# Optimization experiments

Hardware: AMD Instinct MI355X
Metric: run time of the kernel (lower is better)

The kernel has to match this reference:

```python
import jax, jax.numpy as jnp
import numpy as np

N, E, D, T = 50000, 800000, 64, 4
FI = D // T   # per-tower input features (divide_input=True)
FO = D // T   # per-tower output features (output_dim // towers)
NAGG, NSC = 4, 3  # mean/min/max/std ; identity/amplification/attenuation
AVG_LOG = float(np.log(17.0))  # from deg histogram: all nodes have degree 16


def setup_inputs() -> dict:
    key = jax.random.key(0)
    ks = jax.random.split(key, 12)
    rn = lambda k, s: jax.random.normal(k, s, dtype=jnp.float32) * 0.1
    z = lambda s: jnp.zeros(s, jnp.float32)
    post_in = (1 + NAGG * NSC) * FI  # cat([x, scaled aggregations]) per tower
    return {
        "x": jax.random.normal(ks[0], (N, D), dtype=jnp.float32),
        "edge_index": jax.random.randint(ks[1], (2, E), 0, N),
        "alpha": jnp.full((1,), 0.5, dtype=jnp.float32),
        "lin_self_W": rn(ks[2], (D, D)), "lin_self_b": z((D,)),
        "pre_W_s2d": rn(ks[3], (T, 2 * FI, FI)), "pre_b_s2d": z((T, FI)),
        "post_W_s2d": rn(ks[4], (T, post_in, FO)), "post_b_s2d": z((T, FO)),
        "lin_W_s2d": rn(ks[5], (T * FO, D)), "lin_b_s2d": z((D,)),
        "pre_W_d2s": rn(ks[6], (T, 2 * FI, FI)), "pre_b_d2s": z((T, FI)),
        "post_W_d2s": rn(ks[7], (T, post_in, FO)), "post_b_d2s": z((T, FO)),
        "lin_W_d2s": rn(ks[8], (T * FO, D)), "lin_b_d2s": z((D,)),
    }


def _pna(x, recv, send, preW, preb, postW, postb, linW, linb):
    """One PNAConv: messages from `send` nodes aggregated at `recv` nodes."""
    n = x.shape[0]
    xt = x.reshape(n, T, FI)
    # message: per tower cat(x_i, x_j) -> single pre layer (pre_layers=1)
    h = jnp.concatenate([xt[recv], xt[send]], axis=-1)          # [E, T, 2*FI]
    m = jnp.einsum('etf,tfg->etg', h, preW) + preb              # [E, T, FI]
    # aggregators: mean, min, max, std (scatter-reduce over receiver)
    cnt = jax.ops.segment_sum(jnp.ones((recv.shape[0],), m.dtype), recv, n)
    deg = jnp.maximum(cnt, 1.0)[:, None, None]                  # clamp(1), as PyG
    mean = jax.ops.segment_sum(m, recv, n) / deg
    mean_sq = jax.ops.segment_sum(m * m, recv, n) / deg
    std = jnp.sqrt(jnp.maximum(mean_sq - mean * mean, 0.0) + 1e-5)
    has = (cnt > 0.0)[:, None, None]
    mn = jnp.where(has, jax.ops.segment_min(m, recv, n), 0.0)
    mx = jnp.where(has, jax.ops.segment_max(m, recv, n), 0.0)
    agg = jnp.concatenate([mean, mn, mx, std], axis=-1)         # [n, T, 4*FI]
    # degree scalers: identity, amplification, attenuation
    amp = jnp.log(deg + 1.0) / AVG_LOG
    out = jnp.concatenate([agg, agg * amp, agg / amp], axis=-1)  # [n, T, 12*FI]
    out = jnp.concatenate([xt, out], axis=-1)                   # [n, T, 13*FI]
    out = jnp.einsum('ntf,tfg->ntg', out, postW) + postb        # [n, T, FO]
    return out.reshape(n, T * FO) @ linW + linb                 # [n, D]


def reference(x, edge_index, alpha, lin_self_W, lin_self_b,
              pre_W_s2d, pre_b_s2d, post_W_s2d, post_b_s2d, lin_W_s2d, lin_b_s2d,
              pre_W_d2s, pre_b_d2s, post_W_d2s, post_b_d2s, lin_W_d2s, lin_b_d2s):
    src, dst = edge_index[0], edge_index[1]
    y_self = x @ lin_self_W + lin_self_b
    # flow='source_to_target': x_j = src, aggregated at dst
    y_s2d = _pna(x, dst, src, pre_W_s2d, pre_b_s2d, post_W_s2d, post_b_s2d, lin_W_s2d, lin_b_s2d)
    # flow='target_to_source': x_j = dst, aggregated at src
    y_d2s = _pna(x, src, dst, pre_W_d2s, pre_b_d2s, post_W_d2s, post_b_d2s, lin_W_d2s, lin_b_d2s)
    a = alpha[0]
    return y_self + (1.0 - a) * y_s2d + a * y_d2s
```

## Files before the change

### kernel.cpp

```cpp
#include <hip/hip_runtime.h>
#include <math.h>


typedef _Float16 half_t;
typedef __attribute__((ext_vector_type(8))) _Float16 half8;
typedef __attribute__((ext_vector_type(2))) _Float16 half2v;
typedef __attribute__((ext_vector_type(4))) float f32x4;

#define FCAP 12288

static __device__ __forceinline__ unsigned pkmin(unsigned a, unsigned b) {
    unsigned r;
    asm("v_pk_min_f16 %0, %1, %2" : "=v"(r) : "v"(a), "v"(b));
    return r;
}
static __device__ __forceinline__ unsigned pkmax(unsigned a, unsigned b) {
    unsigned r;
    asm("v_pk_max_f16 %0, %1, %2" : "=v"(r) : "v"(a), "v"(b));
    return r;
}
static __device__ __forceinline__ int h2i(half2v h) { return __builtin_bit_cast(int, h); }
static __device__ __forceinline__ half2v u2h(unsigned i) { return __builtin_bit_cast(half2v, i); }
static __device__ __forceinline__ half2v pkrtz(float a, float b) {
    return __builtin_bit_cast(half2v, __builtin_amdgcn_cvt_pkrtz(a, b));
}

__global__ __launch_bounds__(256) void k_pre(
    const int* __restrict__ ei, int nE, int nN,
    int* __restrict__ histD, int* __restrict__ histS,
    const float* __restrict__ postW1, const float* __restrict__ postW2,
    const float* __restrict__ linW1, const float* __restrict__ linW2,
    const float* __restrict__ Wself, const float* __restrict__ bself,
    const float* __restrict__ linb1, const float* __restrict__ linb2,
    const float* __restrict__ postb1, const float* __restrict__ postb2,
    const float* __restrict__ alpha,
    half_t* __restrict__ WLg, half_t* __restrict__ WfinTg, float* __restrict__ bfin,
    const float* __restrict__ x,
    const float* __restrict__ preW1, const float* __restrict__ preW2,
    const float* __restrict__ preb1, const float* __restrict__ preb2,
    half_t* __restrict__ P1, half_t* __restrict__ P2,
    half_t* __restrict__ Q1, half_t* __restrict__ Q2, half_t* __restrict__ xh) {
    int tid = threadIdx.x;
    int b = blockIdx.x;
    if (b < 256) {
        __shared__ int hD[256], hS[256];
        hD[tid] = 0; hS[tid] = 0;
        __syncthreads();
        int chunk = (nE + 255) >> 8;
        int lo = b * chunk;
        int hi = lo + chunk; if (hi > nE) hi = nE;
        for (int e = lo + tid; e < hi; e += 256) {
            int s = ei[e], d = ei[nE + e];
            atomicAdd(&hD[d >> 8], 1);
            atomicAdd(&hS[s >> 8], 1);
        }
        __syncthreads();
        histD[tid * 256 + b] = hD[tid];
        histS[tid * 256 + b] = hS[tid];
    } else if (b < 320) {
        const float a = alpha[0];
        int id = (b - 256) * 256 + tid;
        const int stride = 64 * 256;
        for (int i = id; i < 24 * 16 * 72; i += stride) {
            int m = i / (16 * 72);
            int r = i % (16 * 72);
            int go = r / 72, k = r % 72;
            int d = m / 12, t = (m / 3) % 4, mat = m % 3;
            float v = 0.f;
            if (k < 64) {
                int stat = k >> 4, g = k & 15;
                int basep = (mat == 0) ? 1 : (mat == 1 ? 5 : 9);
                const float* pw = d ? postW2 : postW1;
                v = pw[t * 3328 + ((basep + stat) * 16 + g) * 16 + go];
            }
            WLg[i] = (half_t)v;
        }
        for (int i = id; i < 64 * 192; i += stride) {
            int o = i / 192, k = i % 192;
            float v;
            if (k < 64)       v = (1.f - a) * linW1[k * 64 + o];
            else if (k < 128) v = a * linW2[(k - 64) * 64 + o];
            else {
                int kx = k - 128, t = kx >> 4, f = kx & 15;
                v = Wself[kx * 64 + o];
                float s1 = 0.f, s2 = 0.f;
                for (int go = 0; go < 16; ++go) {
                    s1 += postW1[t * 3328 + f * 16 + go] * linW1[(t * 16 + go) * 64 + o];
                    s2 += postW2[t * 3328 + f * 16 + go] * linW2[(t * 16 + go) * 64 + o];
                }
                v += (1.f - a) * s1 + a * s2;
            }
            WfinTg[i] = (half_t)v;
        }
        for (int i = id; i < 64; i += stride) {
            float v = bself[i] + (1.f - a) * linb1[i] + a * linb2[i];
            for (int j = 0; j < 64; ++j)
                v += (1.f - a) * postb1[j] * linW1[j * 64 + i]
                   + a * postb2[j] * linW2[j * 64 + i];
            bfin[i] = v;
        }
    } else {
        int vb = b - 320;
        const int lane = tid & 63;
        const int t = lane >> 4, g = lane & 15;
        const int base = t << 4;
        float wsP1[16], wsP2[16], wsQ1[16], wsQ2[16];
#pragma unroll
        for (int f = 0; f < 16; ++f) {
            wsP1[f] = preW1[t * 512 + (16 + f) * 16 + g];
            wsP2[f] = preW2[t * 512 + (16 + f) * 16 + g];
            wsQ1[f] = preW1[t * 512 + f * 16 + g];
            wsQ2[f] = preW2[t * 512 + f * 16 + g];
        }
        const float pb1 = preb1[lane], pb2 = preb2[lane];
        int node = (vb * 256 + tid) >> 6;
        const int stride = (768 * 256) >> 6;
        for (; node < nN; node += stride) {
            float xv = x[(size_t)node * 64 + lane];
            float p1 = 0.f, p2 = 0.f, q1 = pb1, q2 = pb2;
#pragma unroll
            for (int f = 0; f < 16; ++f) {
                float v = __shfl(xv, base + f, 64);
                p1 = fmaf(v, wsP1[f], p1);
                p2 = fmaf(v, wsP2[f], p2);
                q1 = fmaf(v, wsQ1[f], q1);
                q2 = fmaf(v, wsQ2[f], q2);
            }
            size_t o = (size_t)node * 64 + lane;
            P1[o] = (half_t)p1;
            P2[o] = (half_t)p2;
            Q1[o] = (half_t)q1;
            Q2[o] = (half_t)q2;
            xh[o] = (half_t)xv;
        }
    }
}

__global__ __launch_bounds__(256) void k_scanA(
    const int* __restrict__ cnt0, const int* __restrict__ cnt1,
    int* __restrict__ off0, int* __restrict__ off1,
    int* __restrict__ bsum, int n, int nchunk) {
    int arr = blockIdx.x >= nchunk;
    int c = blockIdx.x - (arr ? nchunk : 0);
    const int* cnt = arr ? cnt1 : cnt0;
    int* off = arr ? off1 : off0;
    int tid = threadIdx.x;
    int base = c * 1024 + tid * 4;
    int v[4];
#pragma unroll
    for (int k = 0; k < 4; ++k) { int i = base + k; v[k] = (i < n) ? cnt[i] : 0; }
    int tsum = v[0] + v[1] + v[2] + v[3];
    int lane = tid & 63, wid = tid >> 6;
    int incl = tsum;
#pragma unroll
    for (int d = 1; d < 64; d <<= 1) {
        int t = __shfl_up(incl, d, 64);
        if (lane >= d) incl += t;
    }
    __shared__ int ws[4];
    if (lane == 63) ws[wid] = incl;
    __syncthreads();
    int wpre = 0;
    for (int ww = 0; ww < wid; ++ww) wpre += ws[ww];
    int e = wpre + incl - tsum;
#pragma unroll
    for (int k = 0; k < 4; ++k) { int i = base + k; if (i < n) off[i] = e; e += v[k]; }
    if (tid == 255) bsum[blockIdx.x] = wpre + incl;
}

__global__ __launch_bounds__(256) void k_scanB(
    int* __restrict__ off0, int* __restrict__ off1,
    const int* __restrict__ bsum, int n, int nchunk) {
    int arr = blockIdx.x >= nchunk;
    int c = blockIdx.x - (arr ? nchunk : 0);
    int* off = arr ? off1 : off0;
    const int* bs = bsum + (arr ? nchunk : 0);
    __shared__ int pre_s, tot_s;
    int tid = threadIdx.x;
    if (tid < 64) {
        int v = (tid < nchunk) ? bs[tid] : 0;
        int incl = v;
#pragma unroll
        for (int d = 1; d < 64; d <<= 1) {
            int t = __shfl_up(incl, d, 64);
            if (tid >= d) incl += t;
        }
        if (tid == c) pre_s = incl - v;
        if (tid == nchunk - 1) tot_s = incl;
    }
    __syncthreads();
    int pre = pre_s;
    int base = c * 1024 + tid * 4;
#pragma unroll
    for (int k = 0; k < 4; ++k) {
        int i = base + k;
        if (i < n) off[i] += pre;
    }
    if (c == 0 && tid == 0) off[n] = tot_s;
}

__global__ __launch_bounds__(256) void k_bin(
    const int* __restrict__ ei, int nE, int nbuck,
    const int* __restrict__ curD, const int* __restrict__ curS,
    unsigned* __restrict__ binnedD, unsigned* __restrict__ binnedS) {
    __shared__ int cD[256], cS[256];
    int tid = threadIdx.x;
    int hb = blockIdx.x;
    if (tid < nbuck) {
        cD[tid] = curD[tid * 256 + hb];
        cS[tid] = curS[tid * 256 + hb];
    }
    __syncthreads();
    int chunk = (nE + 255) >> 8;
    int lo = hb * chunk;
    int hi = lo + chunk; if (hi > nE) hi = nE;
    for (int e = lo + tid; e < hi; e += 256) {
        int s = ei[e], d = ei[nE + e];
        unsigned pk = (unsigned)s | ((unsigned)d << 16);
        int p = atomicAdd(&cD[d >> 8], 1);
        binnedD[p] = pk;
        int q = atomicAdd(&cS[s >> 8], 1);
        binnedS[q] = pk;
    }
}

__global__ __launch_bounds__(256) void k_fine(
    const unsigned* __restrict__ binnedD, const unsigned* __restrict__ binnedS,
    const int* __restrict__ curD, const int* __restrict__ curS,
    int* __restrict__ off_dst, int* __restrict__ off_src,
    unsigned short* __restrict__ adj_dst, unsigned short* __restrict__ adj_src,
    int nE, int nN, int nbuck) {
    int bk = blockIdx.x;
    int dd = 0;
    if (bk >= nbuck) { dd = 1; bk -= nbuck; }
    const unsigned* binned = dd ? binnedS : binnedD;
    const int* cur = dd ? curS : curD;
    int* off = dd ? off_src : off_dst;
    unsigned short* adj = dd ? adj_src : adj_dst;
    __shared__ int ncnt[256];
    __shared__ int cur2[256];
    __shared__ unsigned short stage[FCAP];
    int tid = threadIdx.x;
    ncnt[tid] = 0;
    __syncthreads();
    int base = cur[bk * 256];
    int endp = cur[(bk + 1) * 256];
    int cntE = endp - base;
    int n0 = bk << 8;
    for (int i = tid; i < cntE; i += 256) {
        unsigned pk = binned[base + i];
        int key = dd ? (int)(pk & 0xFFFFu) : (int)(pk >> 16);
        atomicAdd(&ncnt[key - n0], 1);
    }
    __syncthreads();
    if (tid < 64) {
        int i4 = tid << 2;
        int v0 = ncnt[i4], v1 = ncnt[i4 + 1], v2 = ncnt[i4 + 2], v3 = ncnt[i4 + 3];
        int tsum = v0 + v1 + v2 + v3;
        int incl = tsum;
#pragma unroll
        for (int d = 1; d < 64; d <<= 1) {
            int t = __shfl_up(incl, d, 64);
            if (tid >= d) incl += t;
        }
        int excl = incl - tsum;
        ncnt[i4] = excl;
        ncnt[i4 + 1] = excl + v0;
        ncnt[i4 + 2] = excl + v0 + v1;
        ncnt[i4 + 3] = excl + v0 + v1 + v2;
    }
    __syncthreads();
    cur2[tid] = ncnt[tid];
    int node = n0 + tid;
    if (node < nN) off[node] = base + ncnt[tid];
    if (bk == nbuck - 1 && tid == 0) off[nN] = nE;
    __syncthreads();
    for (int i = tid; i < cntE; i += 256) {
        unsigned pk = binned[base + i];
        int key = dd ? (int)(pk & 0xFFFFu) : (int)(pk >> 16);
        int oth = dd ? (int)(pk >> 16) : (int)(pk & 0xFFFFu);
        int pos = atomicAdd(&cur2[key - n0], 1);
        if (pos < FCAP) stage[pos] = (unsigned short)oth;
        else adj[base + pos] = (unsigned short)oth;
    }
    __syncthreads();
    int lim = cntE < FCAP ? cntE : FCAP;
    for (int i = tid; i < lim; i += 256) adj[base + i] = stage[i];
}

__global__ __launch_bounds__(256) void k_gather(
    const half_t* __restrict__ P1, const half_t* __restrict__ P2,
    const half_t* __restrict__ Q1, const half_t* __restrict__ Q2,
    const int* __restrict__ off1, const unsigned short* __restrict__ adj1,
    const int* __restrict__ off2, const unsigned short* __restrict__ adj2,
    half_t* __restrict__ agg1, half_t* __restrict__ agg2,
    float* __restrict__ amp1, float* __restrict__ ramp1,
    float* __restrict__ amp2, float* __restrict__ ramp2, int nN, int nE) {
    int tid = threadIdx.x;
    const int lane = tid & 63;
    const int g = lane >> 4;
    const int fl = lane & 15;
    const int fl8 = fl << 3;
    int w4 = (blockIdx.x * 256 + tid) >> 6;
    int wstride = (gridDim.x * 256) >> 6;
    int ngroups = (nN + 3) >> 2;
#pragma unroll
    for (int d = 0; d < 2; ++d) {
        const char* Pc = (const char*)(d ? P2 : P1);
        const char* Qc = (const char*)(d ? Q2 : Q1);
        const int* off = d ? off2 : off1;
        const unsigned short* adj = d ? adj2 : adj1;
        char* aggc = (char*)(d ? agg2 : agg1);
        float* ampA = d ? amp2 : amp1;
        float* rampA = d ? ramp2 : ramp1;
        for (int gi = w4; gi < ngroups; gi += wstride) {
            int node = gi * 4 + g;
            bool act = node < nN;
            int nodec = act ? node : (nN - 1);
            int beg = off[nodec], end = off[nodec + 1];
            int cnt = end - beg;
            half2v s01 = {(half_t)0, (half_t)0}, s23 = {(half_t)0, (half_t)0};
            half2v ss01 = {(half_t)0, (half_t)0}, ss23 = {(half_t)0, (half_t)0};
            unsigned mn0 = 0x7C007C00u, mn1 = 0x7C007C00u;
            unsigned mx0 = 0xFC00FC00u, mx1 = 0xFC00FC00u;
            int j = beg;
            for (; j + 4 <= end; j += 4) {
                int n0 = adj[j + 0];
                int n1 = adj[j + 1];
                int n2 = adj[j + 2];
                int n3 = adj[j + 3];
                uint2 u0 = *(const uint2*)(Pc + n0 * 128 + fl8);
                uint2 u1 = *(const uint2*)(Pc + n1 * 128 + fl8);
                uint2 u2 = *(const uint2*)(Pc + n2 * 128 + fl8);
                uint2 u3 = *(const uint2*)(Pc + n3 * 128 + fl8);
                half2v a0 = u2h(u0.x), a1 = u2h(u0.y);
                half2v b0 = u2h(u1.x), b1 = u2h(u1.y);
                half2v c0 = u2h(u2.x), c1 = u2h(u2.y);
                half2v e0 = u2h(u3.x), e1 = u2h(u3.y);
                s01 += (a0 + b0) + (c0 + e0);
                s23 += (a1 + b1) + (c1 + e1);
                ss01 += a0 * a0; ss23 += a1 * a1;
                ss01 += b0 * b0; ss23 += b1 * b1;
                ss01 += c0 * c0; ss23 += c1 * c1;
                ss01 += e0 * e0; ss23 += e1 * e1;
                mn0 = pkmin(mn0, pkmin(pkmin(u0.x, u1.x), pkmin(u2.x, u3.x)));
                mn1 = pkmin(mn1, pkmin(pkmin(u0.y, u1.y), pkmin(u2.y, u3.y)));
                mx0 = pkmax(mx0, pkmax(pkmax(u0.x, u1.x), pkmax(u2.x, u3.x)));
                mx1 = pkmax(mx1, pkmax(pkmax(u0.y, u1.y), pkmax(u2.y, u3.y)));
            }
            for (; j < end; ++j) {
                int n0 = adj[j];
                uint2 u0 = *(const uint2*)(Pc + n0 * 128 + fl8);
                half2v a0 = u2h(u0.x), a1 = u2h(u0.y);
                s01 += a0; s23 += a1;
                ss01 += a0 * a0; ss23 += a1 * a1;
                mn0 = pkmin(mn0, u0.x); mn1 = pkmin(mn1, u0.y);
                mx0 = pkmax(mx0, u0.x); mx1 = pkmax(mx1, u0.y);
            }
            float deg = (cnt > 0) ? (float)cnt : 1.0f;
            float inv = 1.0f / deg;
            float se0 = (float)s01[0], se1 = (float)s01[1];
            float se2 = (float)s23[0], se3 = (float)s23[1];
            float sq0 = (float)ss01[0], sq1 = (float)ss01[1];
            float sq2 = (float)ss23[0], sq3 = (float)ss23[1];
            float me0 = se0 * inv, me1 = se1 * inv, me2 = se2 * inv, me3 = se3 * inv;
            float st0 = sqrtf(fmaxf(fmaf(-me0, me0, sq0 * inv), 0.f) + 1e-5f);
            float st1 = sqrtf(fmaxf(fmaf(-me1, me1, sq1 * inv), 0.f) + 1e-5f);
            float st2 = sqrtf(fmaxf(fmaf(-me2, me2, sq2 * inv), 0.f) + 1e-5f);
            float st3 = sqrtf(fmaxf(fmaf(-me3, me3, sq3 * inv), 0.f) + 1e-5f);
            uint2 qu = *(const uint2*)(Qc + nodec * 128 + fl8);
            half2v q01 = u2h(qu.x), q23 = u2h(qu.y);
            half2v hm01, hm23, hl01, hl23, hh01, hh23;
            if (cnt > 0) {
                hm01 = q01 + pkrtz(me0, me1);
                hm23 = q23 + pkrtz(me2, me3);
                hl01 = q01 + u2h(mn0); hl23 = q23 + u2h(mn1);
                hh01 = q01 + u2h(mx0); hh23 = q23 + u2h(mx1);
            } else {
                half2v z = {(half_t)0, (half_t)0};
                hm01 = z; hm23 = z; hl01 = z; hl23 = z; hh01 = z; hh23 = z;
            }
            half2v hs01 = pkrtz(st0, st1);
            half2v hs23 = pkrtz(st2, st3);
            if (act) {
                char* ab = aggc + (size_t)node * 512 + (fl >> 2) * 128 + (fl & 3) * 8;
                uint2 w0; w0.x = (unsigned)h2i(hm01); w0.y = (unsigned)h2i(hm23);
                uint2 w1; w1.x = (unsigned)h2i(hl01); w1.y = (unsigned)h2i(hl23);
                uint2 w2; w2.x = (unsigned)h2i(hh01); w2.y = (unsigned)h2i(hh23);
                uint2 w3; w3.x = (unsigned)h2i(hs01); w3.y = (unsigned)h2i(hs23);
                *(uint2*)(ab)      = w0;
                *(uint2*)(ab + 32) = w1;
                *(uint2*)(ab + 64) = w2;
                *(uint2*)(ab + 96) = w3;
                if (fl == 0) {
                    float ampv = __log2f(deg + 1.0f) * 0.24465054f;
                    ampA[node] = ampv;
                    rampA[node] = 1.0f / ampv;
                }
            }
        }
    }
}

__global__ __launch_bounds__(256, 2) void k_c(
    const half_t* __restrict__ xh,
    const half_t* __restrict__ agg1, const half_t* __restrict__ agg2,
    const float* __restrict__ amp1, const float* __restrict__ ramp1,
    const float* __restrict__ amp2, const float* __restrict__ ramp2,
    const half_t* __restrict__ WLg, const half_t* __restrict__ WfinT,
    const float* __restrict__ bfin, float* __restrict__ out, int nN) {
    __shared__ half_t WLs[24 * 16 * 72];
    __shared__ half_t osb[4 * 16 * 72];
    int tid = threadIdx.x;
    {
        const uint4* src = (const uint4*)WLg;
        uint4* dst = (uint4*)WLs;
        for (int i = tid; i < (24 * 16 * 72) / 8; i += 256) dst[i] = src[i];
    }
    __syncthreads();
    int w = tid >> 6, lane = tid & 63;
    int l15 = lane & 15, g4 = lane >> 4;
    half_t* ow = osb + w * (16 * 72) + l15 * 72;
    half8 wfr[4][6];
#pragma unroll
    for (int ct = 0; ct < 4; ++ct)
#pragma unroll
        for (int kk = 0; kk < 6; ++kk)
            wfr[ct][kk] = *(const half8*)(WfinT + (ct * 16 + l15) * 192 + kk * 32 + g4 * 8);
    float4 bf4[4];
#pragma unroll
    for (int ct = 0; ct < 4; ++ct)
        bf4[ct] = *(const float4*)(bfin + ct * 16 + g4 * 4);
    int nwaves = gridDim.x * 4;
    int wgid = blockIdx.x * 4 + w;
    int ntiles = (nN + 15) >> 4;
    for (int tile = wgid; tile < ntiles; tile += nwaves) {
        int nrow = (tile << 4) + l15;
        int nrowc = (nrow < nN) ? nrow : (nN - 1);
        half8 xbf[2];
#pragma unroll
        for (int ks = 0; ks < 2; ++ks)
            xbf[ks] = *(const half8*)(xh + (size_t)nrowc * 64 + ks * 32 + g4 * 8);
        f32x4 accY[4] = {{0,0,0,0},{0,0,0,0},{0,0,0,0},{0,0,0,0}};
#pragma unroll
        for (int d = 0; d < 2; ++d) {
            const half_t* agg = d ? agg2 : agg1;
            float ampv = (d ? amp2 : amp1)[nrowc];
            float rampv = (d ? ramp2 : ramp1)[nrowc];
#pragma unroll
            for (int t = 0; t < 4; ++t) {
                half8 b0 = *(const half8*)(agg + (size_t)nrowc * 256 + t * 64 + g4 * 8);
                half8 b1 = *(const half8*)(agg + (size_t)nrowc * 256 + t * 64 + 32 + g4 * 8);
                const half_t* wb = WLs + ((d * 12 + t * 3) * 16 + l15) * 72 + g4 * 8;
                half8 aA0 = *(const half8*)(wb);
                half8 aA1 = *(const half8*)(wb + 32);
                half8 aB0 = *(const half8*)(wb + 16 * 72);
                half8 aB1 = *(const half8*)(wb + 16 * 72 + 32);
                half8 aE0 = *(const half8*)(wb + 32 * 72);
                half8 aE1 = *(const half8*)(wb + 32 * 72 + 32);
                f32x4 zA = {0,0,0,0}, zB = {0,0,0,0}, zE = {0,0,0,0};
                zA = __builtin_amdgcn_mfma_f32_16x16x32_f16(aA0, b0, zA, 0, 0, 0);
                zA = __builtin_amdgcn_mfma_f32_16x16x32_f16(aA1, b1, zA, 0, 0, 0);
                zB = __builtin_amdgcn_mfma_f32_16x16x32_f16(aB0, b0, zB, 0, 0, 0);
                zB = __builtin_amdgcn_mfma_f32_16x16x32_f16(aB1, b1, zB, 0, 0, 0);
                zE = __builtin_amdgcn_mfma_f32_16x16x32_f16(aE0, b0, zE, 0, 0, 0);
                zE = __builtin_amdgcn_mfma_f32_16x16x32_f16(aE1, b1, zE, 0, 0, 0);
                float o0 = zA[0] + ampv * zB[0] + rampv * zE[0];
                float o1 = zA[1] + ampv * zB[1] + rampv * zE[1];
                float o2 = zA[2] + ampv * zB[2] + rampv * zE[2];
                float o3 = zA[3] + ampv * zB[3] + rampv * zE[3];
                half2v p0; p0[0] = (half_t)o0; p0[1] = (half_t)o1;
                half2v p1; p1[0] = (half_t)o2; p1[1] = (half_t)o3;
                *(half2v*)(ow + t * 16 + g4 * 4) = p0;
                *(half2v*)(ow + t * 16 + g4 * 4 + 2) = p1;
            }
#pragma unroll
            for (int ks = 0; ks < 2; ++ks) {
                half8 ob = *(const half8*)(ow + ks * 32 + g4 * 8);
#pragma unroll
                for (int ct = 0; ct < 4; ++ct)
                    accY[ct] = __builtin_amdgcn_mfma_f32_16x16x32_f16(wfr[ct][d * 2 + ks], ob, accY[ct], 0, 0, 0);
            }
        }
#pragma unroll
        for (int ks = 0; ks < 2; ++ks)
#pragma unroll
            for (int ct = 0; ct < 4; ++ct)
                accY[ct] = __builtin_amdgcn_mfma_f32_16x16x32_f16(wfr[ct][4 + ks], xbf[ks], accY[ct], 0, 0, 0);
        if (nrow < nN) {
#pragma unroll
            for (int ct = 0; ct < 4; ++ct) {
                float4 st;
                st.x = accY[ct][0] + bf4[ct].x;
                st.y = accY[ct][1] + bf4[ct].y;
                st.z = accY[ct][2] + bf4[ct].z;
                st.w = accY[ct][3] + bf4[ct].w;
                *(float4*)(out + (size_t)nrow * 64 + ct * 16 + g4 * 4) = st;
            }
        }
    }
}

extern "C" void kernel_launch(void* const* d_in, const int* in_sizes, int n_in,
                              void* d_out, int out_size, void* d_ws, size_t ws_size,
                              hipStream_t stream) {
    const float* x      = (const float*)d_in[0];
    const int*   ei     = (const int*)d_in[1];
    const float* alpha  = (const float*)d_in[2];
    const float* Wself  = (const float*)d_in[3];
    const float* bself  = (const float*)d_in[4];
    const float* preW1  = (const float*)d_in[5];
    const float* preb1  = (const float*)d_in[6];
    const float* postW1 = (const float*)d_in[7];
    const float* postb1 = (const float*)d_in[8];
    const float* linW1  = (const float*)d_in[9];
    const float* linb1  = (const float*)d_in[10];
    const float* preW2  = (const float*)d_in[11];
    const float* preb2  = (const float*)d_in[12];
    const float* postW2 = (const float*)d_in[13];
    const float* postb2 = (const float*)d_in[14];
    const float* linW2  = (const float*)d_in[15];
    const float* linb2  = (const float*)d_in[16];
    float* out = (float*)d_out;
    const int nN = in_sizes[0] / 64;
    const int nE = in_sizes[1] / 2;
    const int nbuck = (nN + 255) >> 8;
    const int nH = nbuck * 256;
    const int nchunk = (nH + 1023) >> 10;

    char* w = (char*)d_ws;
    size_t ofs = 0;
    auto alloc = [&](size_t bytes) {
        char* p = w + ofs;
        ofs = (ofs + bytes + 255) & ~(size_t)255;
        return p;
    };
    half_t* P1   = (half_t*)alloc((size_t)nN * 64 * 2);
    half_t* P2   = (half_t*)alloc((size_t)nN * 64 * 2);
    half_t* Q1   = (half_t*)alloc((size_t)nN * 64 * 2);
    half_t* Q2   = (half_t*)alloc((size_t)nN * 64 * 2);
    half_t* xh   = (half_t*)alloc((size_t)nN * 64 * 2);
    half_t* agg1 = (half_t*)alloc((size_t)nN * 256 * 2);
    half_t* agg2 = (half_t*)alloc((size_t)nN * 256 * 2);
    float* amp1  = (float*)alloc((size_t)nN * 4);
    float* ramp1 = (float*)alloc((size_t)nN * 4);
    float* amp2  = (float*)alloc((size_t)nN * 4);
    float* ramp2 = (float*)alloc((size_t)nN * 4);
    half_t* WLg   = (half_t*)alloc(24 * 16 * 72 * 2);
    half_t* WfinT = (half_t*)alloc(64 * 192 * 2);
    float* bfin   = (float*)alloc(64 * 4);
    int* histD = (int*)alloc(256 * 256 * 4);
    int* histS = (int*)alloc(256 * 256 * 4);
    int* curD  = (int*)alloc((256 * 256 + 1) * 4);
    int* curS  = (int*)alloc((256 * 256 + 1) * 4);
    unsigned* binnedD = (unsigned*)alloc((size_t)nE * 4);
    unsigned* binnedS = (unsigned*)alloc((size_t)nE * 4);
    int* off_dst = (int*)alloc((size_t)(nN + 1) * 4);
    int* off_src = (int*)alloc((size_t)(nN + 1) * 4);
    unsigned short* adj_dst = (unsigned short*)alloc((size_t)nE * 2);
    unsigned short* adj_src = (unsigned short*)alloc((size_t)nE * 2);
    int* bsum = (int*)alloc(2 * 64 * 4);

    k_pre<<<1088, 256, 0, stream>>>(ei, nE, nN, histD, histS,
                                    postW1, postW2, linW1, linW2, Wself, bself,
                                    linb1, linb2, postb1, postb2, alpha,
                                    WLg, WfinT, bfin,
                                    x, preW1, preW2, preb1, preb2,
                                    P1, P2, Q1, Q2, xh);
    k_scanA<<<2 * nchunk, 256, 0, stream>>>(histD, histS, curD, curS, bsum, nH, nchunk);
    k_scanB<<<2 * nchunk, 256, 0, stream>>>(curD, curS, bsum, nH, nchunk);
    k_bin<<<256, 256, 0, stream>>>(ei, nE, nbuck, curD, curS, binnedD, binnedS);
    k_fine<<<2 * nbuck, 256, 0, stream>>>(binnedD, binnedS, curD, curS,
                                          off_dst, off_src, adj_dst, adj_src,
                                          nE, nN, nbuck);
    k_gather<<<2048, 256, 0, stream>>>(P1, P2, Q1, Q2, off_dst, adj_dst, off_src, adj_src,
                                       agg1, agg2, amp1, ramp1, amp2, ramp2, nN, nE);
    k_c<<<512, 256, 0, stream>>>(xh, agg1, agg2, amp1, ramp1, amp2, ramp2,
                                 WLg, WfinT, bfin, out, nN);
}
```

Before: 138.7 us.

## Fuse neighbor gather/aggregation with the post-MLP MFMA kernel via LDS tiles

Merges the gather/aggregate kernel and the post-layer MFMA kernel into one kernel. Each block aggregates 64 nodes into an LDS tile, then runs the per-tower post and final linear matmuls directly from LDS. This removes the global round-trip of the fp16 aggregation buffers and degree scalers, plus one launch. In exchange, weights are read from global memory instead of a persistent LDS copy, grids are non-persistent, and barriers serialize the gather and matmul phases within each block.

```diff
diff --git a/kernel.cpp b/kernel.cpp
--- a/kernel.cpp
+++ b/kernel.cpp
@@ -34,7 +34,7 @@
     const float* __restrict__ linb1, const float* __restrict__ linb2,
     const float* __restrict__ postb1, const float* __restrict__ postb2,
     const float* __restrict__ alpha,
-    half_t* __restrict__ WLg, half_t* __restrict__ WfinTg, float* __restrict__ bfin,
+    half_t* __restrict__ WL2, half_t* __restrict__ WfinTg, float* __restrict__ bfin,
     const float* __restrict__ x,
     const float* __restrict__ preW1, const float* __restrict__ preW2,
     const float* __restrict__ preb1, const float* __restrict__ preb2,
@@ -61,19 +61,15 @@
         const float a = alpha[0];
         int id = (b - 256) * 256 + tid;
         const int stride = 64 * 256;
-        for (int i = id; i < 24 * 16 * 72; i += stride) {
-            int m = i / (16 * 72);
-            int r = i % (16 * 72);
-            int go = r / 72, k = r % 72;
+        for (int i = id; i < 24 * 16 * 64; i += stride) {
+            int m = i / (16 * 64);
+            int r = i % (16 * 64);
+            int go = r / 64, k = r % 64;
             int d = m / 12, t = (m / 3) % 4, mat = m % 3;
-            float v = 0.f;
-            if (k < 64) {
-                int stat = k >> 4, g = k & 15;
-                int basep = (mat == 0) ? 1 : (mat == 1 ? 5 : 9);
-                const float* pw = d ? postW2 : postW1;
-                v = pw[t * 3328 + ((basep + stat) * 16 + g) * 16 + go];
-            }
-            WLg[i] = (half_t)v;
+            int stat = k >> 4, g = k & 15;
+            int basep = (mat == 0) ? 1 : (mat == 1 ? 5 : 9);
+            const float* pw = d ? postW2 : postW1;
+            WL2[i] = (half_t)pw[t * 3328 + ((basep + stat) * 16 + g) * 16 + go];
         }
         for (int i = id; i < 64 * 192; i += stride) {
             int o = i / 192, k = i % 192;
@@ -288,35 +284,35 @@
     for (int i = tid; i < lim; i += 256) adj[base + i] = stage[i];
 }
 
-__global__ __launch_bounds__(256) void k_gather(
+__global__ __launch_bounds__(256, 3) void k_gc(
+    const half_t* __restrict__ xh,
     const half_t* __restrict__ P1, const half_t* __restrict__ P2,
     const half_t* __restrict__ Q1, const half_t* __restrict__ Q2,
     const int* __restrict__ off1, const unsigned short* __restrict__ adj1,
     const int* __restrict__ off2, const unsigned short* __restrict__ adj2,
-    half_t* __restrict__ agg1, half_t* __restrict__ agg2,
-    float* __restrict__ amp1, float* __restrict__ ramp1,
-    float* __restrict__ amp2, float* __restrict__ ramp2, int nN, int nE) {
+    const half_t* __restrict__ WL2, const half_t* __restrict__ WfinT,
+    const float* __restrict__ bfin, float* __restrict__ out, int nN) {
+    __shared__ half_t tileL[64 * 264];
+    __shared__ half_t osb[4 * 16 * 72];
+    __shared__ float ampL[2][64], rampL[2][64];
     int tid = threadIdx.x;
-    const int lane = tid & 63;
-    const int g = lane >> 4;
-    const int fl = lane & 15;
-    const int fl8 = fl << 3;
-    int w4 = (blockIdx.x * 256 + tid) >> 6;
-    int wstride = (gridDim.x * 256) >> 6;
-    int ngroups = (nN + 3) >> 2;
-#pragma unroll
-    for (int d = 0; d < 2; ++d) {
+    int w = tid >> 6, lane = tid & 63;
+    int l15 = lane & 15, g4 = lane >> 4;
+    int gg = tid >> 4, fl = tid & 15;
+    int fl8 = fl << 3;
+    int tb = blockIdx.x * 64;
+    f32x4 accY[4] = {{0,0,0,0},{0,0,0,0},{0,0,0,0},{0,0,0,0}};
+
+    auto GATHER = [&](int d) {
         const char* Pc = (const char*)(d ? P2 : P1);
         const char* Qc = (const char*)(d ? Q2 : Q1);
         const int* off = d ? off2 : off1;
         const unsigned short* adj = d ? adj2 : adj1;
-        char* aggc = (char*)(d ? agg2 : agg1);
-        float* ampA = d ? amp2 : amp1;
-        float* rampA = d ? ramp2 : ramp1;
-        for (int gi = w4; gi < ngroups; gi += wstride) {
-            int node = gi * 4 + g;
-            bool act = node < nN;
-            int nodec = act ? node : (nN - 1);
+#pragma unroll
+        for (int p = 0; p < 4; ++p) {
+            int nl = p * 16 + gg;
+            int node = tb + nl;
+            int nodec = (node < nN) ? node : (nN - 1);
             int beg = off[nodec], end = off[nodec + 1];
             int cnt = end - beg;
             half2v s01 = {(half_t)0, (half_t)0}, s23 = {(half_t)0, (half_t)0};
@@ -382,121 +378,95 @@
             }
             half2v hs01 = pkrtz(st0, st1);
             half2v hs23 = pkrtz(st2, st3);
-            if (act) {
-                char* ab = aggc + (size_t)node * 512 + (fl >> 2) * 128 + (fl & 3) * 8;
-                uint2 w0; w0.x = (unsigned)h2i(hm01); w0.y = (unsigned)h2i(hm23);
-                uint2 w1; w1.x = (unsigned)h2i(hl01); w1.y = (unsigned)h2i(hl23);
-                uint2 w2; w2.x = (unsigned)h2i(hh01); w2.y = (unsigned)h2i(hh23);
-                uint2 w3; w3.x = (unsigned)h2i(hs01); w3.y = (unsigned)h2i(hs23);
-                *(uint2*)(ab)      = w0;
-                *(uint2*)(ab + 32) = w1;
-                *(uint2*)(ab + 64) = w2;
-                *(uint2*)(ab + 96) = w3;
-                if (fl == 0) {
-                    float ampv = __log2f(deg + 1.0f) * 0.24465054f;
-                    ampA[node] = ampv;
-                    rampA[node] = 1.0f / ampv;
-                }
-            }
-        }
-    }
-}
-
-__global__ __launch_bounds__(256, 2) void k_c(
-    const half_t* __restrict__ xh,
-    const half_t* __restrict__ agg1, const half_t* __restrict__ agg2,
-    const float* __restrict__ amp1, const float* __restrict__ ramp1,
-    const float* __restrict__ amp2, const float* __restrict__ ramp2,
-    const half_t* __restrict__ WLg, const half_t* __restrict__ WfinT,
-    const float* __restrict__ bfin, float* __restrict__ out, int nN) {
-    __shared__ half_t WLs[24 * 16 * 72];
-    __shared__ half_t osb[4 * 16 * 72];
-    int tid = threadIdx.x;
-    {
-        const uint4* src = (const uint4*)WLg;
-        uint4* dst = (uint4*)WLs;
-        for (int i = tid; i < (24 * 16 * 72) / 8; i += 256) dst[i] = src[i];
-    }
-    __syncthreads();
-    int w = tid >> 6, lane = tid & 63;
-    int l15 = lane & 15, g4 = lane >> 4;
-    half_t* ow = osb + w * (16 * 72) + l15 * 72;
-    half8 wfr[4][6];
-#pragma unroll
-    for (int ct = 0; ct < 4; ++ct)
-#pragma unroll
-        for (int kk = 0; kk < 6; ++kk)
-            wfr[ct][kk] = *(const half8*)(WfinT + (ct * 16 + l15) * 192 + kk * 32 + g4 * 8);
-    float4 bf4[4];
-#pragma unroll
-    for (int ct = 0; ct < 4; ++ct)
-        bf4[ct] = *(const float4*)(bfin + ct * 16 + g4 * 4);
-    int nwaves = gridDim.x * 4;
-    int wgid = blockIdx.x * 4 + w;
-    int ntiles = (nN + 15) >> 4;
-    for (int tile = wgid; tile < ntiles; tile += nwaves) {
-        int nrow = (tile << 4) + l15;
-        int nrowc = (nrow < nN) ? nrow : (nN - 1);
-        half8 xbf[2];
-#pragma unroll
-        for (int ks = 0; ks < 2; ++ks)
-            xbf[ks] = *(const half8*)(xh + (size_t)nrowc * 64 + ks * 32 + g4 * 8);
-        f32x4 accY[4] = {{0,0,0,0},{0,0,0,0},{0,0,0,0},{0,0,0,0}};
-#pragma unroll
-        for (int d = 0; d < 2; ++d) {
-            const half_t* agg = d ? agg2 : agg1;
-            float ampv = (d ? amp2 : amp1)[nrowc];
-            float rampv = (d ? ramp2 : ramp1)[nrowc];
-#pragma unroll
-            for (int t = 0; t < 4; ++t) {
-                half8 b0 = *(const half8*)(agg + (size_t)nrowc * 256 + t * 64 + g4 * 8);
-                half8 b1 = *(const half8*)(agg + (size_t)nrowc * 256 + t * 64 + 32 + g4 * 8);
-                const half_t* wb = WLs + ((d * 12 + t * 3) * 16 + l15) * 72 + g4 * 8;
-                half8 aA0 = *(const half8*)(wb);
-                half8 aA1 = *(const half8*)(wb + 32);
-                half8 aB0 = *(const half8*)(wb + 16 * 72);
-                half8 aB1 = *(const half8*)(wb + 16 * 72 + 32);
-                half8 aE0 = *(const half8*)(wb + 32 * 72);
-                half8 aE1 = *(const half8*)(wb + 32 * 72 + 32);
-                f32x4 zA = {0,0,0,0}, zB = {0,0,0,0}, zE = {0,0,0,0};
-                zA = __builtin_amdgcn_mfma_f32_16x16x32_f16(aA0, b0, zA, 0, 0, 0);
-                zA = __builtin_amdgcn_mfma_f32_16x16x32_f16(aA1, b1, zA, 0, 0, 0);
-                zB = __builtin_amdgcn_mfma_f32_16x16x32_f16(aB0, b0, zB, 0, 0, 0);
-                zB = __builtin_amdgcn_mfma_f32_16x16x32_f16(aB1, b1, zB, 0, 0, 0);
-                zE = __builtin_amdgcn_mfma_f32_16x16x32_f16(aE0, b0, zE, 0, 0, 0);
-                zE = __builtin_amdgcn_mfma_f32_16x16x32_f16(aE1, b1, zE, 0, 0, 0);
-                float o0 = zA[0] + ampv * zB[0] + rampv * zE[0];
-                float o1 = zA[1] + ampv * zB[1] + rampv * zE[1];
-                float o2 = zA[2] + ampv * zB[2] + rampv * zE[2];
-                float o3 = zA[3] + ampv * zB[3] + rampv * zE[3];
-                half2v p0; p0[0] = (half_t)o0; p0[1] = (half_t)o1;
-                half2v p1; p1[0] = (half_t)o2; p1[1] = (half_t)o3;
-                *(half2v*)(ow + t * 16 + g4 * 4) = p0;
-                *(half2v*)(ow + t * 16 + g4 * 4 + 2) = p1;
-            }
-#pragma unroll
-            for (int ks = 0; ks < 2; ++ks) {
-                half8 ob = *(const half8*)(ow + ks * 32 + g4 * 8);
-#pragma unroll
-                for (int ct = 0; ct < 4; ++ct)
-                    accY[ct] = __builtin_amdgcn_mfma_f32_16x16x32_f16(wfr[ct][d * 2 + ks], ob, accY[ct], 0, 0, 0);
-            }
-        }
-#pragma unroll
-        for (int ks = 0; ks < 2; ++ks)
-#pragma unroll
-            for (int ct = 0; ct < 4; ++ct)
-                accY[ct] = __builtin_amdgcn_mfma_f32_16x16x32_f16(wfr[ct][4 + ks], xbf[ks], accY[ct], 0, 0, 0);
-        if (nrow < nN) {
+            half_t* ab = tileL + nl * 264 + (fl >> 2) * 64 + (fl & 3) * 4;
+            uint2 w0; w0.x = (unsigned)h2i(hm01); w0.y = (unsigned)h2i(hm23);
+            uint2 w1; w1.x = (unsigned)h2i(hl01); w1.y = (unsigned)h2i(hl23);
+            uint2 w2; w2.x = (unsigned)h2i(hh01); w2.y = (unsigned)h2i(hh23);
+            uint2 w3; w3.x = (unsigned)h2i(hs01); w3.y = (unsigned)h2i(hs23);
+            *(uint2*)(ab)      = w0;
+            *(uint2*)(ab + 16) = w1;
+            *(uint2*)(ab + 32) = w2;
+            *(uint2*)(ab + 48) = w3;
+            if (fl == 0) {
+                float ampv = __log2f(deg + 1.0f) * 0.24465054f;
+                ampL[d][nl] = ampv;
+                rampL[d][nl] = 1.0f / ampv;
+            }
+        }
+    };
+
+    auto MPHASE = [&](int d) {
+        half_t* ow = osb + w * (16 * 72) + l15 * 72;
+        float ampv = ampL[d][w * 16 + l15];
+        float rampv = rampL[d][w * 16 + l15];
+        const half_t* trow = tileL + (w * 16 + l15) * 264;
+#pragma unroll
+        for (int t = 0; t < 4; ++t) {
+            half8 b0 = *(const half8*)(trow + t * 64 + g4 * 8);
+            half8 b1 = *(const half8*)(trow + t * 64 + 32 + g4 * 8);
+            const half_t* wb = WL2 + ((d * 12 + t * 3) * 16 + l15) * 64 + g4 * 8;
+            half8 aA0 = *(const half8*)(wb);
+            half8 aA1 = *(const half8*)(wb + 32);
+            half8 aB0 = *(const half8*)(wb + 1024);
+            half8 aB1 = *(const half8*)(wb + 1024 + 32);
+            half8 aE0 = *(const half8*)(wb + 2048);
+            half8 aE1 = *(const half8*)(wb + 2048 + 32);
+            f32x4 zA = {0,0,0,0}, zB = {0,0,0,0}, zE = {0,0,0,0};
+            zA = __builtin_amdgcn_mfma_f32_16x16x32_f16(aA0, b0, zA, 0, 0, 0);
+            zA = __builtin_amdgcn_mfma_f32_16x16x32_f16(aA1, b1, zA, 0, 0, 0);
+            zB = __builtin_amdgcn_mfma_f32_16x16x32_f16(aB0, b0, zB, 0, 0, 0);
+            zB = __builtin_amdgcn_mfma_f32_16x16x32_f16(aB1, b1, zB, 0, 0, 0);
+            zE = __builtin_amdgcn_mfma_f32_16x16x32_f16(aE0, b0, zE, 0, 0, 0);
+            zE = __builtin_amdgcn_mfma_f32_16x16x32_f16(aE1, b1, zE, 0, 0, 0);
+            float o0 = zA[0] + ampv * zB[0] + rampv * zE[0];
+            float o1 = zA[1] + ampv * zB[1] + rampv * zE[1];
+            float o2 = zA[2] + ampv * zB[2] + rampv * zE[2];
+            float o3 = zA[3] + ampv * zB[3] + rampv * zE[3];
+            half2v p0; p0[0] = (half_t)o0; p0[1] = (half_t)o1;
+            half2v p1; p1[0] = (half_t)o2; p1[1] = (half_t)o3;
+            *(half2v*)(ow + t * 16 + g4 * 4) = p0;
+            *(half2v*)(ow + t * 16 + g4 * 4 + 2) = p1;
+        }
+#pragma unroll
+        for (int ks = 0; ks < 2; ++ks) {
+            half8 ob = *(const half8*)(ow + ks * 32 + g4 * 8);
 #pragma unroll
             for (int ct = 0; ct < 4; ++ct) {
-                float4 st;
-                st.x = accY[ct][0] + bf4[ct].x;
-                st.y = accY[ct][1] + bf4[ct].y;
-                st.z = accY[ct][2] + bf4[ct].z;
-                st.w = accY[ct][3] + bf4[ct].w;
-                *(float4*)(out + (size_t)nrow * 64 + ct * 16 + g4 * 4) = st;
-            }
+                half8 af = *(const half8*)(WfinT + (ct * 16 + l15) * 192 + d * 64 + ks * 32 + g4 * 8);
+                accY[ct] = __builtin_amdgcn_mfma_f32_16x16x32_f16(af, ob, accY[ct], 0, 0, 0);
+            }
+        }
+    };
+
+    GATHER(0);
+    __syncthreads();
+    MPHASE(0);
+    __syncthreads();
+    GATHER(1);
+    __syncthreads();
+    MPHASE(1);
+
+    int nrow = tb + w * 16 + l15;
+    int nrowc = (nrow < nN) ? nrow : (nN - 1);
+#pragma unroll
+    for (int ks = 0; ks < 2; ++ks) {
+        half8 xbf = *(const half8*)(xh + (size_t)nrowc * 64 + ks * 32 + g4 * 8);
+#pragma unroll
+        for (int ct = 0; ct < 4; ++ct) {
+            half8 af = *(const half8*)(WfinT + (ct * 16 + l15) * 192 + 128 + ks * 32 + g4 * 8);
+            accY[ct] = __builtin_amdgcn_mfma_f32_16x16x32_f16(af, xbf, accY[ct], 0, 0, 0);
+        }
+    }
+    if (nrow < nN) {
+#pragma unroll
+        for (int ct = 0; ct < 4; ++ct) {
+            float4 bf = *(const float4*)(bfin + ct * 16 + g4 * 4);
+            float4 st;
+            st.x = accY[ct][0] + bf.x;
+            st.y = accY[ct][1] + bf.y;
+            st.z = accY[ct][2] + bf.z;
+            st.w = accY[ct][3] + bf.w;
+            *(float4*)(out + (size_t)nrow * 64 + ct * 16 + g4 * 4) = st;
         }
     }
 }
@@ -540,13 +510,7 @@
     half_t* Q1   = (half_t*)alloc((size_t)nN * 64 * 2);
     half_t* Q2   = (half_t*)alloc((size_t)nN * 64 * 2);
     half_t* xh   = (half_t*)alloc((size_t)nN * 64 * 2);
-    half_t* agg1 = (half_t*)alloc((size_t)nN * 256 * 2);
-    half_t* agg2 = (half_t*)alloc((size_t)nN * 256 * 2);
-    float* amp1  = (float*)alloc((size_t)nN * 4);
-    float* ramp1 = (float*)alloc((size_t)nN * 4);
-    float* amp2  = (float*)alloc((size_t)nN * 4);
-    float* ramp2 = (float*)alloc((size_t)nN * 4);
-    half_t* WLg   = (half_t*)alloc(24 * 16 * 72 * 2);
+    half_t* WL2   = (half_t*)alloc(24 * 16 * 64 * 2);
     half_t* WfinT = (half_t*)alloc(64 * 192 * 2);
     float* bfin   = (float*)alloc(64 * 4);
     int* histD = (int*)alloc(256 * 256 * 4);
@@ -564,7 +528,7 @@
     k_pre<<<1088, 256, 0, stream>>>(ei, nE, nN, histD, histS,
                                     postW1, postW2, linW1, linW2, Wself, bself,
                                     linb1, linb2, postb1, postb2, alpha,
-                                    WLg, WfinT, bfin,
+                                    WL2, WfinT, bfin,
                                     x, preW1, preW2, preb1, preb2,
                                     P1, P2, Q1, Q2, xh);
     k_scanA<<<2 * nchunk, 256, 0, stream>>>(histD, histS, curD, curS, bsum, nH, nchunk);
@@ -573,8 +537,7 @@
     k_fine<<<2 * nbuck, 256, 0, stream>>>(binnedD, binnedS, curD, curS,
                                           off_dst, off_src, adj_dst, adj_src,
                                           nE, nN, nbuck);
-    k_gather<<<2048, 256, 0, stream>>>(P1, P2, Q1, Q2, off_dst, adj_dst, off_src, adj_src,
-                                       agg1, agg2, amp1, ramp1, amp2, ramp2, nN, nE);
-    k_c<<<512, 256, 0, stream>>>(xh, agg1, agg2, amp1, ramp1, amp2, ramp2,
-                                 WLg, WfinT, bfin, out, nN);
-}
+    k_gc<<<(nN + 63) / 64, 256, 0, stream>>>(xh, P1, P2, Q1, Q2,
+                                             off_dst, adj_dst, off_src, adj_src,
+                                             WL2, WfinT, bfin, out, nN);
+}
```

Result: slower. 177.4 us (+27.8%).
